# Performance work log

Measured on AMD Instinct MI355X. Metric: run time of the kernel, lower is better.

The kernel has to match this reference:

```python
import jax, jax.numpy as jnp
import numpy as np

EPS_TOTAL = 1e-6
EPS_LOG = 1e-7


def setup_inputs() -> dict:
    key = jax.random.key(0)
    k1, k2 = jax.random.split(key)
    z = jax.random.normal(k1, (16, 4096, 64), dtype=jnp.float32)
    codebook = jax.random.normal(k2, (1024, 64), dtype=jnp.float32)
    return {"z": z, "codebook": codebook}


def reference(z, codebook):
    # z: [B, T, C]; codebook: [K, C]. Eval-mode forward (mask=None).
    B, T, C = z.shape
    K = codebook.shape[0]
    x = z.reshape(-1, C)  # [N, C]

    # quantize: squared-distance matrix via matmul + argmin (fp32 math)
    d = ((x * x).sum(-1, keepdims=True)
         - 2.0 * (x @ codebook.T)
         + (codebook * codebook).sum(-1)[None, :])  # [N, K]
    code_idx = jnp.argmin(d, axis=-1)  # [N]

    # dequantize: gather codewords
    z_q = codebook[code_idx]  # [N, C]

    # commitment loss: MSE to detached codewords, mean over tokens
    per_tok = ((x - jax.lax.stop_gradient(z_q)) ** 2).mean(-1)  # [N]
    commit_loss = per_tok.mean()

    # straight-through estimator
    z_q_bar = x + jax.lax.stop_gradient(z_q - x)

    # compute_perplexity metrics (eval path): one-hot scatter histogram
    counts = jnp.zeros((K,), dtype=x.dtype).at[code_idx].add(1.0)
    total = jnp.maximum(counts.sum(), EPS_TOTAL)
    prob = counts / total
    ppl = jnp.exp(-(prob * jnp.log(prob + EPS_LOG)).sum())
    usage = (counts >= 1.0).astype(x.dtype).mean()

    return z_q_bar.reshape(B, T, C), commit_loss, ppl, usage
```

## Files before the change

### kernel.cpp

```cpp
#include <hip/hip_runtime.h>


typedef _Float16 half8 __attribute__((ext_vector_type(8)));
typedef float f32x4 __attribute__((ext_vector_type(4)));

#define NTOK 65536
#define KCODE 1024
#define OUT_SCALARS 4194304
#define MARGIN 1e-3f

#define WS_CNT   1024
#define WS_LOSS  2048
#define WS_CBHL  20480

static __device__ __forceinline__ unsigned int order_key(float f) {
    unsigned int u = __float_as_uint(f);
    unsigned int mask = (u >> 31) ? 0xFFFFFFFFu : 0x80000000u;
    return u ^ mask;
}
static __device__ __forceinline__ float key_to_float(unsigned int k) {
    unsigned int u = (k & 0x80000000u) ? (k ^ 0x80000000u) : ~k;
    return __uint_as_float(u);
}
static __device__ __forceinline__ unsigned long long umin64(unsigned long long a,
                                                            unsigned long long b) {
    return a < b ? a : b;
}
static __device__ __forceinline__ unsigned long long umax64(unsigned long long a,
                                                            unsigned long long b) {
    return a > b ? a : b;
}

__global__ void prep_kernel(const float* __restrict__ cb, float* __restrict__ ws) {
    const int k = blockIdx.x * 256 + threadIdx.x;
    const float4* cb4 = (const float4*)cb;
    float s = 0.f;
#pragma unroll
    for (int j = 0; j < 16; ++j) {
        float4 v = cb4[k * 16 + j];
        s = fmaf(v.x, v.x, s);
        s = fmaf(v.y, v.y, s);
        s = fmaf(v.z, v.z, s);
        s = fmaf(v.w, v.w, s);
    }
    ws[k] = s;
    ws[WS_CNT + k] = 0.f;

    _Float16* base = (_Float16*)(ws + WS_CBHL) + (size_t)(k >> 4) * 2048 + (k & 15) * 64;
    const int c = k & 15;
#pragma unroll
    for (int d8 = 0; d8 < 8; ++d8) {
        float4 a = cb4[k * 16 + 2 * d8], b = cb4[k * 16 + 2 * d8 + 1];
        float xf[8] = {a.x, a.y, a.z, a.w, b.x, b.y, b.z, b.w};
        half8 h, lo;
#pragma unroll
        for (int i = 0; i < 8; ++i) {
            _Float16 hi = (_Float16)xf[i];
            h[i] = hi;
            lo[i] = (_Float16)((xf[i] - (float)hi) * 4096.f);
        }
        const int pos = ((d8 + c) & 7) * 8;
        *(half8*)(base + pos) = h;
        *(half8*)(base + 1024 + pos) = lo;
    }
}

__launch_bounds__(256, 3)
__global__ void quant_kernel(const float* __restrict__ z,
                             const float* __restrict__ cb,
                             float* __restrict__ out,
                             float* __restrict__ ws) {
    const int t = threadIdx.x, blk = blockIdx.x;
    const int w = t >> 6, l = t & 63;
    const int cl = l & 15, g = l >> 4;
    const int tok0 = blk * 64;
    const int tokL = w * 16 + cl;
    const int tokG = tok0 + tokL;

    __shared__ __align__(16) _Float16 ring[4][3][2048];
    __shared__ __align__(16) float cn_lds[1024];
    __shared__ int win[64];
    __shared__ float lsum[64];

    *(float4*)&cn_lds[t * 4] = *(const float4*)(ws + t * 4);

    half8 zh[2], zl[2];
    {
        const float4* z4 = (const float4*)z + (size_t)tokG * 16;
#pragma unroll
        for (int q = 0; q < 2; ++q) {
            float4 a = z4[2 * g + 8 * q], b = z4[2 * g + 8 * q + 1];
            float xf[8] = {a.x, a.y, a.z, a.w, b.x, b.y, b.z, b.w};
#pragma unroll
            for (int i = 0; i < 8; ++i) {
                _Float16 h = (_Float16)xf[i];
                zh[q][i] = h;
                zl[q][i] = (_Float16)((xf[i] - (float)h) * 4096.f);
            }
        }
    }

    asm volatile("s_waitcnt vmcnt(0) lgkmcnt(0)" ::: "memory");
    __builtin_amdgcn_sched_barrier(0);
    __syncthreads();

    const char* dma_src = (const char*)(ws + WS_CBHL) + l * 16;
    const int rot = (g + cl) & 7;
    const int o0 = cl * 64 + rot * 8;
    const int o1 = cl * 64 + (rot ^ 4) * 8;

#pragma unroll
    for (int p = 0; p < 2; ++p)
#pragma unroll
        for (int q = 0; q < 4; ++q)
            __builtin_amdgcn_global_load_lds(
                (const __attribute__((address_space(1))) void*)(dma_src + p * 4096 + q * 1024),
                (__attribute__((address_space(3))) void*)&ring[w][p][q * 512], 16, 0, 0);

    float d1 = 3.4e38f, d2 = 3.4e38f;
    int idx1 = 0, idx2 = 0;

#define TILE_BODY(ti, SLOT, VM, ISSUE)                                                \
    {                                                                                 \
        asm volatile("s_waitcnt vmcnt(" VM ")" ::: "memory");                         \
        const _Float16* tp = &ring[w][SLOT][0];                                       \
        half8 H0 = *(const half8*)(tp + o0);                                          \
        half8 H1 = *(const half8*)(tp + o1);                                          \
        half8 L0 = *(const half8*)(tp + 1024 + o0);                                   \
        half8 L1 = *(const half8*)(tp + 1024 + o1);                                   \
        float4 cnv = *(const float4*)&cn_lds[(ti) * 16 + 4 * g];                      \
        const float cna[4] = {cnv.x, cnv.y, cnv.z, cnv.w};                            \
        if (ISSUE) {                                                                  \
            _Pragma("unroll")                                                         \
            for (int q = 0; q < 4; ++q)                                               \
                __builtin_amdgcn_global_load_lds(                                     \
                    (const __attribute__((address_space(1))) void*)(dma_src + ((ti) + 2) * 4096 + q * 1024), \
                    (__attribute__((address_space(3))) void*)&ring[w][((SLOT) + 2) % 3][q * 512], \
                    16, 0, 0);                                                        \
        }                                                                             \
        f32x4 a1 = {0.f,0.f,0.f,0.f}, a2 = {0.f,0.f,0.f,0.f};                         \
        a1 = __builtin_amdgcn_mfma_f32_16x16x32_f16(H0, zh[0], a1, 0, 0, 0);          \
        a1 = __builtin_amdgcn_mfma_f32_16x16x32_f16(H1, zh[1], a1, 0, 0, 0);          \
        a2 = __builtin_amdgcn_mfma_f32_16x16x32_f16(H0, zl[0], a2, 0, 0, 0);          \
        a2 = __builtin_amdgcn_mfma_f32_16x16x32_f16(H1, zl[1], a2, 0, 0, 0);          \
        a2 = __builtin_amdgcn_mfma_f32_16x16x32_f16(L0, zh[0], a2, 0, 0, 0);          \
        a2 = __builtin_amdgcn_mfma_f32_16x16x32_f16(L1, zh[1], a2, 0, 0, 0);          \
        _Pragma("unroll")                                                             \
        for (int r = 0; r < 4; ++r) {                                                 \
            float dot = fmaf(a2[r], 2.44140625e-4f, a1[r]);                           \
            float d = fmaf(-2.f, dot, cna[r]);                                        \
            const int kidx = (ti) * 16 + 4 * g + r;                                   \
            bool lt = d < d1;                                                         \
            bool mid = d < d2;                                                        \
            idx2 = lt ? idx1 : (mid ? kidx : idx2);    \
            d2 = fminf(d2, fmaxf(d, d1));                                             \
            idx1 = lt ? kidx : idx1;                                                  \
            d1 = fminf(d1, d);                                                        \
        }                                                                             \
    }

    for (int i3 = 0; i3 < 60; i3 += 3) {
        TILE_BODY(i3 + 0, 0, "4", 1)
        TILE_BODY(i3 + 1, 1, "4", 1)
        TILE_BODY(i3 + 2, 2, "4", 1)
    }
    TILE_BODY(60, 0, "4", 1)
    TILE_BODY(61, 1, "4", 1)
    TILE_BODY(62, 2, "4", 0)
    TILE_BODY(63, 0, "0", 0)
#undef TILE_BODY

    unsigned long long k1 = ((unsigned long long)order_key(d1) << 32) | (unsigned)idx1;
    unsigned long long k2 = ((unsigned long long)order_key(d2) << 32) | (unsigned)idx2;
#pragma unroll
    for (int off = 16; off <= 32; off <<= 1) {
        unsigned long long ok1 = __shfl_xor(k1, off, 64);
        unsigned long long ok2 = __shfl_xor(k2, off, 64);
        unsigned long long lo = umin64(k1, ok1);
        unsigned long long hi = umax64(k1, ok1);
        k2 = umin64(hi, umin64(k2, ok2));
        k1 = lo;
    }

    if (l < 16) {
        int fidx = (int)(unsigned)(k1 & 0xFFFFFFFFull);
        const float d1f = key_to_float((unsigned)(k1 >> 32));
        const float d2f = key_to_float((unsigned)(k2 >> 32));
        if (d2f - d1f < MARGIN) {
            const int ia = fidx;
            const int ib = (int)(unsigned)(k2 & 0xFFFFFFFFull);
            const float4* zr = (const float4*)z + (size_t)tokG * 16;
            const float4* ca = (const float4*)cb + (size_t)ia * 16;
            const float4* cbp = (const float4*)cb + (size_t)ib * 16;
            float sa = 0.f, sb = 0.f;
#pragma unroll
            for (int j = 0; j < 16; ++j) {
                float4 xv = zr[j];
                float4 va = ca[j], vb = cbp[j];
                sa = fmaf(xv.x, va.x, sa); sb = fmaf(xv.x, vb.x, sb);
                sa = fmaf(xv.y, va.y, sa); sb = fmaf(xv.y, vb.y, sb);
                sa = fmaf(xv.z, va.z, sa); sb = fmaf(xv.z, vb.z, sb);
                sa = fmaf(xv.w, va.w, sa); sb = fmaf(xv.w, vb.w, sb);
            }
            const float ea = fmaf(-2.f, sa, cn_lds[ia]);
            const float eb = fmaf(-2.f, sb, cn_lds[ib]);
            const unsigned long long ka = ((unsigned long long)order_key(ea) << 32) | (unsigned)ia;
            const unsigned long long kb = ((unsigned long long)order_key(eb) << 32) | (unsigned)ib;
            fidx = (int)(unsigned)(umin64(ka, kb) & 0xFFFFFFFFull);
        }
        win[tokL] = fidx;
        atomicAdd(&ws[WS_CNT + fidx], 1.f);
    }
    __syncthreads();

    {
        const int tokr = t >> 2, fb = (t & 3) * 4;
        const int idx = win[tokr];
        const float4* zr = (const float4*)z + (size_t)(tok0 + tokr) * 16;
        const float4* cq = (const float4*)cb + (size_t)idx * 16;
        float4* o4 = (float4*)out + (size_t)(tok0 + tokr) * 16;
        float ss = 0.f;
#pragma unroll
        for (int j = 0; j < 4; ++j) {
            float4 xv = zr[fb + j];
            float4 qv = cq[fb + j];
            float4 ov; float dx;
            dx = qv.x - xv.x; ov.x = xv.x + dx; ss = fmaf(dx, dx, ss);
            dx = qv.y - xv.y; ov.y = xv.y + dx; ss = fmaf(dx, dx, ss);
            dx = qv.z - xv.z; ov.z = xv.z + dx; ss = fmaf(dx, dx, ss);
            dx = qv.w - xv.w; ov.w = xv.w + dx; ss = fmaf(dx, dx, ss);
            o4[fb + j] = ov;
        }
        ss += __shfl_down(ss, 2, 64);
        ss += __shfl_down(ss, 1, 64);
        if ((t & 3) == 0) lsum[tokr] = ss * (1.f / 64.f);
    }
    __syncthreads();
    if (t < 64) {
        float v = lsum[t];
#pragma unroll
        for (int off = 32; off > 0; off >>= 1) v += __shfl_down(v, off, 64);
        if (t == 0) ws[WS_LOSS + blk] = v;
    }
}

__global__ void final_kernel(const float* __restrict__ ws, float* __restrict__ out) {
    const int t = threadIdx.x;
    const int l = t & 63, wv = t >> 6;
    __shared__ float rbuf[16];

#define BLOCK_REDUCE(VAR, EXPR)                                             \
    float VAR;                                                              \
    {                                                                       \
        float v_ = (EXPR);                                                  \
        _Pragma("unroll")                                                   \
        for (int off = 32; off > 0; off >>= 1) v_ += __shfl_down(v_, off, 64); \
        if (l == 0) rbuf[wv] = v_;                                          \
        __syncthreads();                                                    \
        float r_ = (t < 16) ? rbuf[t] : 0.f;                                \
        if (wv == 0) {                                                      \
            _Pragma("unroll")                                               \
            for (int off = 8; off > 0; off >>= 1) r_ += __shfl_down(r_, off, 64); \
            if (l == 0) rbuf[0] = r_;                                       \
        }                                                                   \
        __syncthreads();                                                    \
        VAR = rbuf[0];                                                      \
        __syncthreads();                                                    \
    }

    const float c = ws[WS_CNT + t];
    BLOCK_REDUCE(totraw, c)
    const float total = fmaxf(totraw, 1e-6f);
    const float p = c / total;
    BLOCK_REDUCE(ent, p * logf(p + 1e-7f))
    BLOCK_REDUCE(used, (c >= 1.f) ? 1.f : 0.f)
    BLOCK_REDUCE(loss, ws[WS_LOSS + t])
#undef BLOCK_REDUCE

    if (t == 0) {
        out[OUT_SCALARS + 0] = loss * (1.f / (float)NTOK);
        out[OUT_SCALARS + 1] = expf(-ent);
        out[OUT_SCALARS + 2] = used * (1.f / (float)KCODE);
    }
}

extern "C" void kernel_launch(void* const* d_in, const int* in_sizes, int n_in,
                              void* d_out, int out_size, void* d_ws, size_t ws_size,
                              hipStream_t stream) {
    const float* z  = (const float*)d_in[0];
    const float* cb = (const float*)d_in[1];
    float* out = (float*)d_out;
    float* ws  = (float*)d_ws;

    prep_kernel <<<4, 256, 0, stream>>>(cb, ws);
    quant_kernel<<<NTOK / 64, 256, 0, stream>>>(z, cb, out, ws);
    final_kernel<<<1, 1024, 0, stream>>>(ws, out);
}
```

Before: 80.31 us.

## Process two 16-token fragments per wave to reuse codebook tiles

Each wave now handles 32 tokens instead of 16, so every codebook tile streamed into LDS and loaded into registers feeds two sets of MFMAs and two argmin trackers. The grid is halved to 512 blocks, and the epilogue, loss reduction and final kernel are adjusted to match. The goal is to halve codebook DMA and LDS read traffic per token and give the MFMA pipe independent chains to interleave. In exchange it raises register pressure (the launch bound of 3 blocks per CU is kept) and leaves fewer blocks to fill the GPU.

```diff
diff --git a/kernel.cpp b/kernel.cpp
--- a/kernel.cpp
+++ b/kernel.cpp
@@ -73,32 +73,37 @@
     const int t = threadIdx.x, blk = blockIdx.x;
     const int w = t >> 6, l = t & 63;
     const int cl = l & 15, g = l >> 4;
-    const int tok0 = blk * 64;
-    const int tokL = w * 16 + cl;
-    const int tokG = tok0 + tokL;
+    const int tok0 = blk * 128;
+    const int tokW = tok0 + w * 32;
+    const int tokA = tokW + cl;
+    const int tokB = tokW + 16 + cl;
 
     __shared__ __align__(16) _Float16 ring[4][3][2048];
     __shared__ __align__(16) float cn_lds[1024];
-    __shared__ int win[64];
-    __shared__ float lsum[64];
+    __shared__ int win[128];
+    __shared__ float lsum[128];
 
     *(float4*)&cn_lds[t * 4] = *(const float4*)(ws + t * 4);
 
-    half8 zh[2], zl[2];
-    {
-        const float4* z4 = (const float4*)z + (size_t)tokG * 16;
-#pragma unroll
-        for (int q = 0; q < 2; ++q) {
-            float4 a = z4[2 * g + 8 * q], b = z4[2 * g + 8 * q + 1];
-            float xf[8] = {a.x, a.y, a.z, a.w, b.x, b.y, b.z, b.w};
-#pragma unroll
-            for (int i = 0; i < 8; ++i) {
-                _Float16 h = (_Float16)xf[i];
-                zh[q][i] = h;
-                zl[q][i] = (_Float16)((xf[i] - (float)h) * 4096.f);
-            }
-        }
-    }
+    half8 zhA[2], zlA[2], zhB[2], zlB[2];
+#define MKFRAG(ZH, ZL, TOK)                                                \
+    {                                                                      \
+        const float4* z4 = (const float4*)z + (size_t)(TOK) * 16;          \
+        _Pragma("unroll")                                                  \
+        for (int q = 0; q < 2; ++q) {                                      \
+            float4 a = z4[2 * g + 8 * q], b = z4[2 * g + 8 * q + 1];       \
+            float xf[8] = {a.x, a.y, a.z, a.w, b.x, b.y, b.z, b.w};        \
+            _Pragma("unroll")                                              \
+            for (int i = 0; i < 8; ++i) {                                  \
+                _Float16 h = (_Float16)xf[i];                              \
+                ZH[q][i] = h;                                              \
+                ZL[q][i] = (_Float16)((xf[i] - (float)h) * 4096.f);        \
+            }                                                              \
+        }                                                                  \
+    }
+    MKFRAG(zhA, zlA, tokA)
+    MKFRAG(zhB, zlB, tokB)
+#undef MKFRAG
 
     asm volatile("s_waitcnt vmcnt(0) lgkmcnt(0)" ::: "memory");
     __builtin_amdgcn_sched_barrier(0);
@@ -117,8 +122,18 @@
                 (const __attribute__((address_space(1))) void*)(dma_src + p * 4096 + q * 1024),
                 (__attribute__((address_space(3))) void*)&ring[w][p][q * 512], 16, 0, 0);
 
-    float d1 = 3.4e38f, d2 = 3.4e38f;
-    int idx1 = 0, idx2 = 0;
+    float d1A = 3.4e38f, d2A = 3.4e38f, d1B = 3.4e38f, d2B = 3.4e38f;
+    int i1A = 0, i2A = 0, i1B = 0, i2B = 0;
+
+#define ARGMIN2(D, KIDX, D1, D2, I1, I2)                                    \
+    {                                                                       \
+        bool lt = (D) < D1;                                                 \
+        bool mid = (D) < D2;                                                \
+        I2 = lt ? I1 : (mid ? (KIDX) : I2);                                 \
+        D2 = fminf(D2, fmaxf((D), D1));                                     \
+        I1 = lt ? (KIDX) : I1;                                              \
+        D1 = fminf(D1, (D));                                                \
+    }
 
 #define TILE_BODY(ti, SLOT, VM, ISSUE)                                                \
     {                                                                                 \
@@ -138,24 +153,29 @@
                     (__attribute__((address_space(3))) void*)&ring[w][((SLOT) + 2) % 3][q * 512], \
                     16, 0, 0);                                                        \
         }                                                                             \
-        f32x4 a1 = {0.f,0.f,0.f,0.f}, a2 = {0.f,0.f,0.f,0.f};                         \
-        a1 = __builtin_amdgcn_mfma_f32_16x16x32_f16(H0, zh[0], a1, 0, 0, 0);          \
-        a1 = __builtin_amdgcn_mfma_f32_16x16x32_f16(H1, zh[1], a1, 0, 0, 0);          \
-        a2 = __builtin_amdgcn_mfma_f32_16x16x32_f16(H0, zl[0], a2, 0, 0, 0);          \
-        a2 = __builtin_amdgcn_mfma_f32_16x16x32_f16(H1, zl[1], a2, 0, 0, 0);          \
-        a2 = __builtin_amdgcn_mfma_f32_16x16x32_f16(L0, zh[0], a2, 0, 0, 0);          \
-        a2 = __builtin_amdgcn_mfma_f32_16x16x32_f16(L1, zh[1], a2, 0, 0, 0);          \
+        f32x4 a1A = {0.f,0.f,0.f,0.f}, a2A = {0.f,0.f,0.f,0.f};                       \
+        f32x4 a1B = {0.f,0.f,0.f,0.f}, a2B = {0.f,0.f,0.f,0.f};                       \
+        a1A = __builtin_amdgcn_mfma_f32_16x16x32_f16(H0, zhA[0], a1A, 0, 0, 0);       \
+        a1B = __builtin_amdgcn_mfma_f32_16x16x32_f16(H0, zhB[0], a1B, 0, 0, 0);       \
+        a1A = __builtin_amdgcn_mfma_f32_16x16x32_f16(H1, zhA[1], a1A, 0, 0, 0);       \
+        a1B = __builtin_amdgcn_mfma_f32_16x16x32_f16(H1, zhB[1], a1B, 0, 0, 0);       \
+        a2A = __builtin_amdgcn_mfma_f32_16x16x32_f16(H0, zlA[0], a2A, 0, 0, 0);       \
+        a2B = __builtin_amdgcn_mfma_f32_16x16x32_f16(H0, zlB[0], a2B, 0, 0, 0);       \
+        a2A = __builtin_amdgcn_mfma_f32_16x16x32_f16(H1, zlA[1], a2A, 0, 0, 0);       \
+        a2B = __builtin_amdgcn_mfma_f32_16x16x32_f16(H1, zlB[1], a2B, 0, 0, 0);       \
+        a2A = __builtin_amdgcn_mfma_f32_16x16x32_f16(L0, zhA[0], a2A, 0, 0, 0);       \
+        a2B = __builtin_amdgcn_mfma_f32_16x16x32_f16(L0, zhB[0], a2B, 0, 0, 0);       \
+        a2A = __builtin_amdgcn_mfma_f32_16x16x32_f16(L1, zhA[1], a2A, 0, 0, 0);       \
+        a2B = __builtin_amdgcn_mfma_f32_16x16x32_f16(L1, zhB[1], a2B, 0, 0, 0);       \
         _Pragma("unroll")                                                             \
         for (int r = 0; r < 4; ++r) {                                                 \
-            float dot = fmaf(a2[r], 2.44140625e-4f, a1[r]);                           \
-            float d = fmaf(-2.f, dot, cna[r]);                                        \
             const int kidx = (ti) * 16 + 4 * g + r;                                   \
-            bool lt = d < d1;                                                         \
-            bool mid = d < d2;                                                        \
-            idx2 = lt ? idx1 : (mid ? kidx : idx2);    \
-            d2 = fminf(d2, fmaxf(d, d1));                                             \
-            idx1 = lt ? kidx : idx1;                                                  \
-            d1 = fminf(d1, d);                                                        \
+            float dotA = fmaf(a2A[r], 2.44140625e-4f, a1A[r]);                        \
+            float dA = fmaf(-2.f, dotA, cna[r]);                                      \
+            ARGMIN2(dA, kidx, d1A, d2A, i1A, i2A)                                     \
+            float dotB = fmaf(a2B[r], 2.44140625e-4f, a1B[r]);                        \
+            float dB = fmaf(-2.f, dotB, cna[r]);                                      \
+            ARGMIN2(dB, kidx, d1B, d2B, i1B, i2B)                                     \
         }                                                                             \
     }
 
@@ -169,75 +189,93 @@
     TILE_BODY(62, 2, "4", 0)
     TILE_BODY(63, 0, "0", 0)
 #undef TILE_BODY
-
-    unsigned long long k1 = ((unsigned long long)order_key(d1) << 32) | (unsigned)idx1;
-    unsigned long long k2 = ((unsigned long long)order_key(d2) << 32) | (unsigned)idx2;
-#pragma unroll
-    for (int off = 16; off <= 32; off <<= 1) {
-        unsigned long long ok1 = __shfl_xor(k1, off, 64);
-        unsigned long long ok2 = __shfl_xor(k2, off, 64);
-        unsigned long long lo = umin64(k1, ok1);
-        unsigned long long hi = umax64(k1, ok1);
-        k2 = umin64(hi, umin64(k2, ok2));
-        k1 = lo;
+#undef ARGMIN2
+
+#define MERGE2(K1, K2)                                                      \
+    _Pragma("unroll")                                                       \
+    for (int off = 16; off <= 32; off <<= 1) {                              \
+        unsigned long long ok1 = __shfl_xor(K1, off, 64);                   \
+        unsigned long long ok2 = __shfl_xor(K2, off, 64);                   \
+        unsigned long long lo = umin64(K1, ok1);                            \
+        unsigned long long hi = umax64(K1, ok1);                            \
+        K2 = umin64(hi, umin64(K2, ok2));                                   \
+        K1 = lo;                                                            \
+    }
+    unsigned long long k1A = ((unsigned long long)order_key(d1A) << 32) | (unsigned)i1A;
+    unsigned long long k2A = ((unsigned long long)order_key(d2A) << 32) | (unsigned)i2A;
+    unsigned long long k1B = ((unsigned long long)order_key(d1B) << 32) | (unsigned)i1B;
+    unsigned long long k2B = ((unsigned long long)order_key(d2B) << 32) | (unsigned)i2B;
+    MERGE2(k1A, k2A)
+    MERGE2(k1B, k2B)
+#undef MERGE2
+
+#define RESOLVE(K1, K2, TOK, FIDX)                                          \
+    int FIDX = (int)(unsigned)(K1 & 0xFFFFFFFFull);                         \
+    {                                                                       \
+        const float d1f = key_to_float((unsigned)(K1 >> 32));               \
+        const float d2f = key_to_float((unsigned)(K2 >> 32));               \
+        if (d2f - d1f < MARGIN) {                                           \
+            const int ia = FIDX;                                            \
+            const int ib = (int)(unsigned)(K2 & 0xFFFFFFFFull);             \
+            const float4* zr = (const float4*)z + (size_t)(TOK) * 16;       \
+            const float4* ca = (const float4*)cb + (size_t)ia * 16;         \
+            const float4* cbp = (const float4*)cb + (size_t)ib * 16;        \
+            float sa = 0.f, sb = 0.f;                                       \
+            _Pragma("unroll")                                               \
+            for (int j = 0; j < 16; ++j) {                                  \
+                float4 xv = zr[j];                                          \
+                float4 va = ca[j], vb = cbp[j];                             \
+                sa = fmaf(xv.x, va.x, sa); sb = fmaf(xv.x, vb.x, sb);       \
+                sa = fmaf(xv.y, va.y, sa); sb = fmaf(xv.y, vb.y, sb);       \
+                sa = fmaf(xv.z, va.z, sa); sb = fmaf(xv.z, vb.z, sb);       \
+                sa = fmaf(xv.w, va.w, sa); sb = fmaf(xv.w, vb.w, sb);       \
+            }                                                               \
+            const float ea = fmaf(-2.f, sa, cn_lds[ia]);                    \
+            const float eb = fmaf(-2.f, sb, cn_lds[ib]);                    \
+            const unsigned long long ka =                                   \
+                ((unsigned long long)order_key(ea) << 32) | (unsigned)ia;   \
+            const unsigned long long kb =                                   \
+                ((unsigned long long)order_key(eb) << 32) | (unsigned)ib;   \
+            FIDX = (int)(unsigned)(umin64(ka, kb) & 0xFFFFFFFFull);         \
+        }                                                                   \
     }
 
     if (l < 16) {
-        int fidx = (int)(unsigned)(k1 & 0xFFFFFFFFull);
-        const float d1f = key_to_float((unsigned)(k1 >> 32));
-        const float d2f = key_to_float((unsigned)(k2 >> 32));
-        if (d2f - d1f < MARGIN) {
-            const int ia = fidx;
-            const int ib = (int)(unsigned)(k2 & 0xFFFFFFFFull);
-            const float4* zr = (const float4*)z + (size_t)tokG * 16;
-            const float4* ca = (const float4*)cb + (size_t)ia * 16;
-            const float4* cbp = (const float4*)cb + (size_t)ib * 16;
-            float sa = 0.f, sb = 0.f;
-#pragma unroll
-            for (int j = 0; j < 16; ++j) {
-                float4 xv = zr[j];
-                float4 va = ca[j], vb = cbp[j];
-                sa = fmaf(xv.x, va.x, sa); sb = fmaf(xv.x, vb.x, sb);
-                sa = fmaf(xv.y, va.y, sa); sb = fmaf(xv.y, vb.y, sb);
-                sa = fmaf(xv.z, va.z, sa); sb = fmaf(xv.z, vb.z, sb);
-                sa = fmaf(xv.w, va.w, sa); sb = fmaf(xv.w, vb.w, sb);
-            }
-            const float ea = fmaf(-2.f, sa, cn_lds[ia]);
-            const float eb = fmaf(-2.f, sb, cn_lds[ib]);
-            const unsigned long long ka = ((unsigned long long)order_key(ea) << 32) | (unsigned)ia;
-            const unsigned long long kb = ((unsigned long long)order_key(eb) << 32) | (unsigned)ib;
-            fidx = (int)(unsigned)(umin64(ka, kb) & 0xFFFFFFFFull);
-        }
-        win[tokL] = fidx;
-        atomicAdd(&ws[WS_CNT + fidx], 1.f);
-    }
+        RESOLVE(k1A, k2A, tokA, fidxA)
+        RESOLVE(k1B, k2B, tokB, fidxB)
+        win[w * 32 + l] = fidxA;
+        win[w * 32 + 16 + l] = fidxB;
+        atomicAdd(&ws[WS_CNT + fidxA], 1.f);
+        atomicAdd(&ws[WS_CNT + fidxB], 1.f);
+    }
+#undef RESOLVE
     __syncthreads();
 
     {
-        const int tokr = t >> 2, fb = (t & 3) * 4;
-        const int idx = win[tokr];
-        const float4* zr = (const float4*)z + (size_t)(tok0 + tokr) * 16;
-        const float4* cq = (const float4*)cb + (size_t)idx * 16;
-        float4* o4 = (float4*)out + (size_t)(tok0 + tokr) * 16;
+        const int lt = t >> 1, h = t & 1;
+        const int tokE = tok0 + lt;
+        const int idx = win[lt];
+        const float4* zr = (const float4*)z + (size_t)tokE * 16 + h * 8;
+        const float4* cq = (const float4*)cb + (size_t)idx * 16 + h * 8;
+        float4* o4 = (float4*)out + (size_t)tokE * 16 + h * 8;
         float ss = 0.f;
 #pragma unroll
-        for (int j = 0; j < 4; ++j) {
-            float4 xv = zr[fb + j];
-            float4 qv = cq[fb + j];
+        for (int j = 0; j < 8; ++j) {
+            float4 xv = zr[j];
+            float4 qv = cq[j];
             float4 ov; float dx;
             dx = qv.x - xv.x; ov.x = xv.x + dx; ss = fmaf(dx, dx, ss);
             dx = qv.y - xv.y; ov.y = xv.y + dx; ss = fmaf(dx, dx, ss);
             dx = qv.z - xv.z; ov.z = xv.z + dx; ss = fmaf(dx, dx, ss);
             dx = qv.w - xv.w; ov.w = xv.w + dx; ss = fmaf(dx, dx, ss);
-            o4[fb + j] = ov;
+            o4[j] = ov;
         }
-        ss += __shfl_down(ss, 2, 64);
-        ss += __shfl_down(ss, 1, 64);
-        if ((t & 3) == 0) lsum[tokr] = ss * (1.f / 64.f);
+        float os = __shfl_down(ss, 1, 64);
+        if (h == 0) lsum[lt] = (ss + os) * (1.f / 64.f);
     }
     __syncthreads();
     if (t < 64) {
-        float v = lsum[t];
+        float v = lsum[t] + lsum[t + 64];
 #pragma unroll
         for (int off = 32; off > 0; off >>= 1) v += __shfl_down(v, off, 64);
         if (t == 0) ws[WS_LOSS + blk] = v;
@@ -274,7 +312,7 @@
     const float p = c / total;
     BLOCK_REDUCE(ent, p * logf(p + 1e-7f))
     BLOCK_REDUCE(used, (c >= 1.f) ? 1.f : 0.f)
-    BLOCK_REDUCE(loss, ws[WS_LOSS + t])
+    BLOCK_REDUCE(loss, (t < 512) ? ws[WS_LOSS + t] : 0.f)
 #undef BLOCK_REDUCE
 
     if (t == 0) {
@@ -293,6 +331,6 @@
     float* ws  = (float*)d_ws;
 
     prep_kernel <<<4, 256, 0, stream>>>(cb, ws);
-    quant_kernel<<<NTOK / 64, 256, 0, stream>>>(z, cb, out, ws);
+    quant_kernel<<<NTOK / 128, 256, 0, stream>>>(z, cb, out, ws);
     final_kernel<<<1, 1024, 0, stream>>>(ws, out);
 }
```

After: 88.51 us. 1.1x slower.

## Add dedicated producer wave that streams codebook tiles into a shared LDS ring

Applied to the files above, without the earlier changes.

Adds a fifth wave per block that acts as a producer. It DMA-loads codebook fp16 hi/lo tiles into a single 8-slot LDS ring shared by the four consumer waves. Previously each consumer wave loaded its own private copy of every tile, which repeated the same global-to-LDS traffic four times. Tile readiness and slot reuse are now tracked with volatile LDS counters, spin-waits with s_sleep, and LDS atomics. This cuts redundant loads and LDS footprint, but adds polling latency and a per-tile handshake dependency on the producer, and raises the block size to 320 threads.

```diff
diff --git a/kernel.cpp b/kernel.cpp
--- a/kernel.cpp
+++ b/kernel.cpp
@@ -65,7 +65,7 @@
     }
 }
 
-__launch_bounds__(256, 3)
+__launch_bounds__(320, 4)
 __global__ void quant_kernel(const float* __restrict__ z,
                              const float* __restrict__ cb,
                              float* __restrict__ out,
@@ -73,19 +73,24 @@
     const int t = threadIdx.x, blk = blockIdx.x;
     const int w = t >> 6, l = t & 63;
     const int cl = l & 15, g = l >> 4;
+    const bool prod = (w == 4);
     const int tok0 = blk * 64;
     const int tokL = w * 16 + cl;
-    const int tokG = tok0 + tokL;
-
-    __shared__ __align__(16) _Float16 ring[4][3][2048];
+    const int tokG = tok0 + (prod ? 0 : tokL);
+
+    __shared__ __align__(16) _Float16 ring[8][2048];
     __shared__ __align__(16) float cn_lds[1024];
     __shared__ int win[64];
     __shared__ float lsum[64];
-
-    *(float4*)&cn_lds[t * 4] = *(const float4*)(ws + t * 4);
+    __shared__ int tiles_ready;
+    __shared__ int consumed[8];
+
+    if (t == 0) tiles_ready = 0;
+    if (t < 8) consumed[t] = 0;
+    if (t < 256) *(float4*)&cn_lds[t * 4] = *(const float4*)(ws + t * 4);
 
     half8 zh[2], zl[2];
-    {
+    if (!prod) {
         const float4* z4 = (const float4*)z + (size_t)tokG * 16;
 #pragma unroll
         for (int q = 0; q < 2; ++q) {
@@ -99,121 +104,126 @@
             }
         }
     }
-
-    asm volatile("s_waitcnt vmcnt(0) lgkmcnt(0)" ::: "memory");
-    __builtin_amdgcn_sched_barrier(0);
     __syncthreads();
-
-    const char* dma_src = (const char*)(ws + WS_CBHL) + l * 16;
-    const int rot = (g + cl) & 7;
-    const int o0 = cl * 64 + rot * 8;
-    const int o1 = cl * 64 + (rot ^ 4) * 8;
-
-#pragma unroll
-    for (int p = 0; p < 2; ++p)
-#pragma unroll
-        for (int q = 0; q < 4; ++q)
-            __builtin_amdgcn_global_load_lds(
-                (const __attribute__((address_space(1))) void*)(dma_src + p * 4096 + q * 1024),
-                (__attribute__((address_space(3))) void*)&ring[w][p][q * 512], 16, 0, 0);
 
     float d1 = 3.4e38f, d2 = 3.4e38f;
     int idx1 = 0, idx2 = 0;
 
-#define TILE_BODY(ti, SLOT, VM, ISSUE)                                                \
-    {                                                                                 \
-        asm volatile("s_waitcnt vmcnt(" VM ")" ::: "memory");                         \
-        const _Float16* tp = &ring[w][SLOT][0];                                       \
-        half8 H0 = *(const half8*)(tp + o0);                                          \
-        half8 H1 = *(const half8*)(tp + o1);                                          \
-        half8 L0 = *(const half8*)(tp + 1024 + o0);                                   \
-        half8 L1 = *(const half8*)(tp + 1024 + o1);                                   \
-        float4 cnv = *(const float4*)&cn_lds[(ti) * 16 + 4 * g];                      \
-        const float cna[4] = {cnv.x, cnv.y, cnv.z, cnv.w};                            \
-        if (ISSUE) {                                                                  \
-            _Pragma("unroll")                                                         \
-            for (int q = 0; q < 4; ++q)                                               \
-                __builtin_amdgcn_global_load_lds(                                     \
-                    (const __attribute__((address_space(1))) void*)(dma_src + ((ti) + 2) * 4096 + q * 1024), \
-                    (__attribute__((address_space(3))) void*)&ring[w][((SLOT) + 2) % 3][q * 512], \
-                    16, 0, 0);                                                        \
-        }                                                                             \
-        f32x4 a1 = {0.f,0.f,0.f,0.f}, a2 = {0.f,0.f,0.f,0.f};                         \
-        a1 = __builtin_amdgcn_mfma_f32_16x16x32_f16(H0, zh[0], a1, 0, 0, 0);          \
-        a1 = __builtin_amdgcn_mfma_f32_16x16x32_f16(H1, zh[1], a1, 0, 0, 0);          \
-        a2 = __builtin_amdgcn_mfma_f32_16x16x32_f16(H0, zl[0], a2, 0, 0, 0);          \
-        a2 = __builtin_amdgcn_mfma_f32_16x16x32_f16(H1, zl[1], a2, 0, 0, 0);          \
-        a2 = __builtin_amdgcn_mfma_f32_16x16x32_f16(L0, zh[0], a2, 0, 0, 0);          \
-        a2 = __builtin_amdgcn_mfma_f32_16x16x32_f16(L1, zh[1], a2, 0, 0, 0);          \
-        _Pragma("unroll")                                                             \
-        for (int r = 0; r < 4; ++r) {                                                 \
-            float dot = fmaf(a2[r], 2.44140625e-4f, a1[r]);                           \
-            float d = fmaf(-2.f, dot, cna[r]);                                        \
-            const int kidx = (ti) * 16 + 4 * g + r;                                   \
-            bool lt = d < d1;                                                         \
-            bool mid = d < d2;                                                        \
-            idx2 = lt ? idx1 : (mid ? kidx : idx2);    \
-            d2 = fminf(d2, fmaxf(d, d1));                                             \
-            idx1 = lt ? kidx : idx1;                                                  \
-            d1 = fminf(d1, d);                                                        \
-        }                                                                             \
-    }
-
-    for (int i3 = 0; i3 < 60; i3 += 3) {
-        TILE_BODY(i3 + 0, 0, "4", 1)
-        TILE_BODY(i3 + 1, 1, "4", 1)
-        TILE_BODY(i3 + 2, 2, "4", 1)
-    }
-    TILE_BODY(60, 0, "4", 1)
-    TILE_BODY(61, 1, "4", 1)
-    TILE_BODY(62, 2, "4", 0)
-    TILE_BODY(63, 0, "0", 0)
-#undef TILE_BODY
-
-    unsigned long long k1 = ((unsigned long long)order_key(d1) << 32) | (unsigned)idx1;
-    unsigned long long k2 = ((unsigned long long)order_key(d2) << 32) | (unsigned)idx2;
-#pragma unroll
-    for (int off = 16; off <= 32; off <<= 1) {
-        unsigned long long ok1 = __shfl_xor(k1, off, 64);
-        unsigned long long ok2 = __shfl_xor(k2, off, 64);
-        unsigned long long lo = umin64(k1, ok1);
-        unsigned long long hi = umax64(k1, ok1);
-        k2 = umin64(hi, umin64(k2, ok2));
-        k1 = lo;
-    }
-
-    if (l < 16) {
-        int fidx = (int)(unsigned)(k1 & 0xFFFFFFFFull);
-        const float d1f = key_to_float((unsigned)(k1 >> 32));
-        const float d2f = key_to_float((unsigned)(k2 >> 32));
-        if (d2f - d1f < MARGIN) {
-            const int ia = fidx;
-            const int ib = (int)(unsigned)(k2 & 0xFFFFFFFFull);
-            const float4* zr = (const float4*)z + (size_t)tokG * 16;
-            const float4* ca = (const float4*)cb + (size_t)ia * 16;
-            const float4* cbp = (const float4*)cb + (size_t)ib * 16;
-            float sa = 0.f, sb = 0.f;
-#pragma unroll
-            for (int j = 0; j < 16; ++j) {
-                float4 xv = zr[j];
-                float4 va = ca[j], vb = cbp[j];
-                sa = fmaf(xv.x, va.x, sa); sb = fmaf(xv.x, vb.x, sb);
-                sa = fmaf(xv.y, va.y, sa); sb = fmaf(xv.y, vb.y, sb);
-                sa = fmaf(xv.z, va.z, sa); sb = fmaf(xv.z, vb.z, sb);
-                sa = fmaf(xv.w, va.w, sa); sb = fmaf(xv.w, vb.w, sb);
+    if (prod) {
+        const char* src = (const char*)(ws + WS_CBHL) + l * 16;
+        volatile int* vcons = consumed;
+        volatile int* vtr = &tiles_ready;
+        for (int T = 0; T < 64; ++T) {
+            const int s = T & 7;
+            if (T >= 8) {
+                const int need = (T >> 3) * 4;
+                while (vcons[s] < need) __builtin_amdgcn_s_sleep(1);
             }
-            const float ea = fmaf(-2.f, sa, cn_lds[ia]);
-            const float eb = fmaf(-2.f, sb, cn_lds[ib]);
-            const unsigned long long ka = ((unsigned long long)order_key(ea) << 32) | (unsigned)ia;
-            const unsigned long long kb = ((unsigned long long)order_key(eb) << 32) | (unsigned)ib;
-            fidx = (int)(unsigned)(umin64(ka, kb) & 0xFFFFFFFFull);
-        }
-        win[tokL] = fidx;
-        atomicAdd(&ws[WS_CNT + fidx], 1.f);
+            __builtin_amdgcn_sched_barrier(0);
+#pragma unroll
+            for (int q = 0; q < 4; ++q)
+                __builtin_amdgcn_global_load_lds(
+                    (const __attribute__((address_space(1))) void*)(src + T * 4096 + q * 1024),
+                    (__attribute__((address_space(3))) void*)&ring[s][q * 512], 16, 0, 0);
+            asm volatile("s_waitcnt vmcnt(16)" ::: "memory");
+            if (l == 0 && T >= 4) *vtr = T - 3;
+        }
+        asm volatile("s_waitcnt vmcnt(8)" ::: "memory");
+        if (l == 0) *vtr = 62;
+        asm volatile("s_waitcnt vmcnt(4)" ::: "memory");
+        if (l == 0) *vtr = 63;
+        asm volatile("s_waitcnt vmcnt(0)" ::: "memory");
+        if (l == 0) *vtr = 64;
+    } else {
+        const int rot = (g + cl) & 7;
+        const int o0 = cl * 64 + rot * 8;
+        const int o1 = cl * 64 + (rot ^ 4) * 8;
+        volatile int* vtr = &tiles_ready;
+
+        for (int T = 0; T < 64; ++T) {
+            while (*vtr < T + 1) __builtin_amdgcn_s_sleep(1);
+            __builtin_amdgcn_sched_barrier(0);
+            const _Float16* tp = &ring[T & 7][0];
+            half8 H0 = *(const half8*)(tp + o0);
+            half8 H1 = *(const half8*)(tp + o1);
+            half8 L0 = *(const half8*)(tp + 1024 + o0);
+            half8 L1 = *(const half8*)(tp + 1024 + o1);
+            float4 cnv = *(const float4*)&cn_lds[T * 16 + 4 * g];
+            __builtin_amdgcn_sched_barrier(0);
+            if (l == 0) atomicAdd(&consumed[T & 7], 1);
+
+            f32x4 a1 = {0.f, 0.f, 0.f, 0.f}, a2 = {0.f, 0.f, 0.f, 0.f};
+            a1 = __builtin_amdgcn_mfma_f32_16x16x32_f16(H0, zh[0], a1, 0, 0, 0);
+            a1 = __builtin_amdgcn_mfma_f32_16x16x32_f16(H1, zh[1], a1, 0, 0, 0);
+            a2 = __builtin_amdgcn_mfma_f32_16x16x32_f16(H0, zl[0], a2, 0, 0, 0);
+            a2 = __builtin_amdgcn_mfma_f32_16x16x32_f16(H1, zl[1], a2, 0, 0, 0);
+            a2 = __builtin_amdgcn_mfma_f32_16x16x32_f16(L0, zh[0], a2, 0, 0, 0);
+            a2 = __builtin_amdgcn_mfma_f32_16x16x32_f16(L1, zh[1], a2, 0, 0, 0);
+
+            const float cna[4] = {cnv.x, cnv.y, cnv.z, cnv.w};
+#pragma unroll
+            for (int r = 0; r < 4; ++r) {
+                float dot = fmaf(a2[r], 2.44140625e-4f, a1[r]);
+                float d = fmaf(-2.f, dot, cna[r]);
+                const int kidx = T * 16 + 4 * g + r;
+                bool lt = d < d1;
+                bool mid = d < d2;
+                idx2 = lt ? idx1 : (mid ? kidx : idx2);
+                d2 = fminf(d2, fmaxf(d, d1));
+                idx1 = lt ? kidx : idx1;
+                d1 = fminf(d1, d);
+            }
+        }
+    }
+
+    if (!prod) {
+        unsigned long long k1 = ((unsigned long long)order_key(d1) << 32) | (unsigned)idx1;
+        unsigned long long k2 = ((unsigned long long)order_key(d2) << 32) | (unsigned)idx2;
+#pragma unroll
+        for (int off = 16; off <= 32; off <<= 1) {
+            unsigned long long ok1 = __shfl_xor(k1, off, 64);
+            unsigned long long ok2 = __shfl_xor(k2, off, 64);
+            unsigned long long lo = umin64(k1, ok1);
+            unsigned long long hi = umax64(k1, ok1);
+            k2 = umin64(hi, umin64(k2, ok2));
+            k1 = lo;
+        }
+
+        if (l < 16) {
+            int fidx = (int)(unsigned)(k1 & 0xFFFFFFFFull);
+            const float d1f = key_to_float((unsigned)(k1 >> 32));
+            const float d2f = key_to_float((unsigned)(k2 >> 32));
+            if (d2f - d1f < MARGIN) {
+                const int ia = fidx;
+                const int ib = (int)(unsigned)(k2 & 0xFFFFFFFFull);
+                const float4* zr = (const float4*)z + (size_t)tokG * 16;
+                const float4* ca = (const float4*)cb + (size_t)ia * 16;
+                const float4* cbp = (const float4*)cb + (size_t)ib * 16;
+                float sa = 0.f, sb = 0.f;
+#pragma unroll
+                for (int j = 0; j < 16; ++j) {
+                    float4 xv = zr[j];
+                    float4 va = ca[j], vb = cbp[j];
+                    sa = fmaf(xv.x, va.x, sa); sb = fmaf(xv.x, vb.x, sb);
+                    sa = fmaf(xv.y, va.y, sa); sb = fmaf(xv.y, vb.y, sb);
+                    sa = fmaf(xv.z, va.z, sa); sb = fmaf(xv.z, vb.z, sb);
+                    sa = fmaf(xv.w, va.w, sa); sb = fmaf(xv.w, vb.w, sb);
+                }
+                const float ea = fmaf(-2.f, sa, cn_lds[ia]);
+                const float eb = fmaf(-2.f, sb, cn_lds[ib]);
+                const unsigned long long ka =
+                    ((unsigned long long)order_key(ea) << 32) | (unsigned)ia;
+                const unsigned long long kb =
+                    ((unsigned long long)order_key(eb) << 32) | (unsigned)ib;
+                fidx = (int)(unsigned)(umin64(ka, kb) & 0xFFFFFFFFull);
+            }
+            win[tokL] = fidx;
+            atomicAdd(&ws[WS_CNT + fidx], 1.f);
+        }
     }
     __syncthreads();
 
-    {
+    if (t < 256) {
         const int tokr = t >> 2, fb = (t & 3) * 4;
         const int idx = win[tokr];
         const float4* zr = (const float4*)z + (size_t)(tok0 + tokr) * 16;
@@ -293,6 +303,6 @@
     float* ws  = (float*)d_ws;
 
     prep_kernel <<<4, 256, 0, stream>>>(cb, ws);
-    quant_kernel<<<NTOK / 64, 256, 0, stream>>>(z, cb, out, ws);
+    quant_kernel<<<NTOK / 64, 320, 0, stream>>>(z, cb, out, ws);
     final_kernel<<<1, 1024, 0, stream>>>(ws, out);
 }
```

Measured after the change: 113.3 us. 1.41x slower.
